# Optimization experiments

Measured on AMD Instinct MI355X. Metric: run time of the kernel, lower is better.

The kernel has to match this reference:

```python
import jax, jax.numpy as jnp
import numpy as np

B, DIM, H, W = 8, 256, 128, 128
HEADS = 4
C = DIM // HEADS  # per-head channels = 64


def conv1x1(x, w):
    # x: [b,c,h,w], w: [o,c] -> [b,o,h,w]
    return jnp.einsum('bchw,oc->bohw', x, w)


def setup_inputs() -> dict:
    key = jax.random.key(0)
    ks = jax.random.split(key, 10)
    d3 = DIM * 3
    return {
        'x': jax.random.normal(ks[0], (B, DIM, H, W), dtype=jnp.float32),
        'w_qkv': jax.random.normal(ks[1], (d3, DIM), dtype=jnp.float32) * (1.0 / np.sqrt(DIM)),
        'w_dw': jax.random.normal(ks[2], (d3, 1, 3, 3), dtype=jnp.float32) * (1.0 / 3.0),
        'temperature': jnp.ones((HEADS, 1, 1), dtype=jnp.float32),
        'attn1': jnp.array([0.2], dtype=jnp.float32),
        'attn2': jnp.array([0.2], dtype=jnp.float32),
        'attn3': jnp.array([0.2], dtype=jnp.float32),
        'attn4': jnp.array([0.2], dtype=jnp.float32),
        'gate_w1': jax.random.normal(ks[3], (DIM // 2, DIM), dtype=jnp.float32) * (1.0 / np.sqrt(DIM)),
        'gate_b1': jnp.zeros((DIM // 2,), dtype=jnp.float32),
        'gate_w2': jax.random.normal(ks[4], (1, DIM // 2), dtype=jnp.float32) * (1.0 / np.sqrt(DIM // 2)),
        'gate_b2': jnp.zeros((1,), dtype=jnp.float32),
    }


def reference(x, w_qkv, w_dw, temperature, attn1, attn2, attn3, attn4,
              gate_w1, gate_b1, gate_w2, gate_b2):
    b, c, h, w = x.shape
    n = h * w
    # qkv: 1x1 conv then 3x3 depthwise conv (groups = 3*dim)
    qkv = conv1x1(x, w_qkv)
    qkv = jax.lax.conv_general_dilated(
        qkv, w_dw, window_strides=(1, 1), padding='SAME',
        feature_group_count=3 * DIM,
        dimension_numbers=('NCHW', 'OIHW', 'NCHW'))
    q, k, v = jnp.split(qkv, 3, axis=1)
    # b (head c) h w -> b head c (h w)
    q = q.reshape(b, HEADS, C, n)
    k = k.reshape(b, HEADS, C, n)
    v = v.reshape(b, HEADS, C, n)
    # L2 normalize along token dim (F.normalize, eps=1e-12)
    q = q / jnp.maximum(jnp.linalg.norm(q, axis=-1, keepdims=True), 1e-12)
    k = k / jnp.maximum(jnp.linalg.norm(k, axis=-1, keepdims=True), 1e-12)
    # gate -> dynamic_k = int(C * mean(sigmoid(...)))
    g = jax.nn.relu(conv1x1(x, gate_w1) + gate_b1[None, :, None, None])
    g = jax.nn.sigmoid(conv1x1(g, gate_w2) + gate_b2[None, :, None, None])
    dk = jnp.clip(jnp.floor(C * jnp.mean(g)).astype(jnp.int32), 1, C)
    # channel attention: [b, heads, C, C]
    attn = jnp.einsum('bhcn,bhdn->bhcd', q, k) * temperature[None]
    # top-k mask: keep entries >= dk-th largest per row (ties negligible)
    vals = jax.lax.top_k(attn, C)[0]  # descending sorted values
    thresh = vals[..., dk - 1][..., None]
    attn = jnp.where(attn >= thresh, attn, -jnp.inf)
    attn = jax.nn.softmax(attn, axis=-1)
    # out1..out4 are identical (attn @ v); dedup into one matmul
    av = jnp.einsum('bhcd,bhdn->bhcn', attn, v)
    out = av * (attn1 + attn2 + attn3 + attn4)
    return out.reshape(b, c, h, w)
```

## Files before the change

kernel.cpp:

```cpp
#include <hip/hip_runtime.h>
#include <hip/hip_bf16.h>
#include <cmath>

#define HW_ 16384
#define IMG_W 128
#define IMG_H 128
#define DIM_ 256
#define D3_ 768
#define HEADS_ 4
#define C_ 64
#define B_ 8

typedef unsigned short ushort_t;
typedef __attribute__((ext_vector_type(8))) short short8v;
typedef __attribute__((ext_vector_type(16))) float f32x16;

#define GLL16(gp, lp) __builtin_amdgcn_global_load_lds( \
    (const __attribute__((address_space(1))) void*)(gp), \
    (__attribute__((address_space(3))) void*)(lp), 16, 0, 0)

static __device__ __forceinline__ ushort_t f2bf_bits(float v) {
  __hip_bfloat16 h = __float2bfloat16(v);
  return *reinterpret_cast<ushort_t*>(&h);
}
static __device__ __forceinline__ float bf2f(ushort_t u) {
  return __uint_as_float(((unsigned int)u) << 16);
}

__global__ __launch_bounds__(256) void k0_wsplit(
    const float* __restrict__ wqkv, const float* __restrict__ gw1,
    ushort_t* __restrict__ WH, ushort_t* __restrict__ WL)
{
  const int row = blockIdx.x;
  const int t = threadIdx.x;
  const float* src = (row < 768) ? (wqkv + (size_t)row * DIM_)
                                 : (gw1 + (size_t)(row - 768) * DIM_);
  const float v = src[t];
  const ushort_t hb = f2bf_bits(v);
  WH[(size_t)row * DIM_ + t] = hb;
  WL[(size_t)row * DIM_ + t] = f2bf_bits(v - bf2f(hb));
}

__global__ __launch_bounds__(256, 2) void k1_mfma(
    const ushort_t* __restrict__ WH, const ushort_t* __restrict__ WL,
    const float* __restrict__ x, const float* __restrict__ gb1,
    const float* __restrict__ gw2, const float* __restrict__ gb2,
    float* __restrict__ qkvraw, float* __restrict__ gpart, int bbase)
{
  const int t = threadIdx.x;
  const int cb = blockIdx.x, rb = blockIdx.y, s = blockIdx.z;
  const int row0 = rb * 128, col0 = cb * 128;
  const float* xb = x + (size_t)(bbase + s) * DIM_ * HW_;

  __shared__ __align__(16) unsigned char lds[65536];
  ushort_t* ldsA = (ushort_t*)lds;
  float*    ldsB = (float*)(lds + 32768);

  const int lane = t & 63, wid = t >> 6;
  const int rr = lane & 31, lh = lane >> 5;

  const size_t arowb = (size_t)(row0 + wid * 32 + rr) * DIM_;

  f32x16 acc[4];
#pragma unroll
  for (int mi = 0; mi < 4; ++mi)
#pragma unroll
    for (int r = 0; r < 16; ++r) acc[mi][r] = 0.f;

  auto STAGE = [&](int pb, int kt) {
    ushort_t* abase = ldsA + pb * 8192;
#pragma unroll
    for (int i = 0; i < 2; ++i) {
      const int koff = kt * 32 + i * 16 + lh * 8;
      ushort_t* dst = abase + (wid * 2 + i) * 512;
      GLL16(WH + arowb + koff, dst);
      GLL16(WL + arowb + koff, dst + 4096);
    }
    float* bbase = ldsB + pb * 4096;
#pragma unroll
    for (int j = 0; j < 4; ++j) {
      const int crow = wid * 8 + j * 2 + lh;
      const float* src = xb + (size_t)(kt * 32 + crow) * HW_ + col0 + rr * 4;
      GLL16(src, bbase + (wid * 8 + j * 2) * 128);
    }
  };

  auto COMPUTE = [&](int pb) {
    const ushort_t* pAH = ldsA + pb * 8192;
    const ushort_t* pAL = pAH + 4096;
    const float* bx = ldsB + pb * 4096;
    const int lo = lane * 8;
    const int pidx = wid * 32 + rr;
#pragma unroll
    for (int ks = 0; ks < 2; ++ks) {
      short8v ah[4], al[4];
#pragma unroll
      for (int mi = 0; mi < 4; ++mi) {
        const int base = mi * 1024 + ks * 512 + lo;
        ah[mi] = *(const short8v*)(pAH + base);
        al[mi] = *(const short8v*)(pAL + base);
      }
      short8v bh, bl;
#pragma unroll
      for (int j = 0; j < 8; ++j) {
        const float fv = bx[(ks * 16 + lh * 8 + j) * 128 + pidx];
        const ushort_t hb = f2bf_bits(fv);
        bh[j] = (short)hb;
        bl[j] = (short)f2bf_bits(fv - bf2f(hb));
      }
#pragma unroll
      for (int mi = 0; mi < 4; ++mi) {
        acc[mi] = __builtin_amdgcn_mfma_f32_32x32x16_bf16(ah[mi], bh, acc[mi], 0, 0, 0);
        acc[mi] = __builtin_amdgcn_mfma_f32_32x32x16_bf16(ah[mi], bl, acc[mi], 0, 0, 0);
        acc[mi] = __builtin_amdgcn_mfma_f32_32x32x16_bf16(al[mi], bh, acc[mi], 0, 0, 0);
      }
    }
  };

  STAGE(0, 0);
  __syncthreads();

  for (int kt = 0; kt < 8; ++kt) {
    const int pb = kt & 1;
    if (kt < 7) STAGE(pb ^ 1, kt + 1);
    COMPUTE(pb);
    __syncthreads();
  }

  const int cl = lane & 31;
  if (rb < 6) {
    const int p = col0 + wid * 32 + cl;
#pragma unroll
    for (int mi = 0; mi < 4; ++mi)
#pragma unroll
      for (int r = 0; r < 16; ++r) {
        const int row = (r & 3) + 8 * (r >> 2) + 4 * lh;
        const int m = row0 + mi * 32 + row;
        qkvraw[((size_t)s * D3_ + m) * HW_ + p] = acc[mi][r];
      }
  } else {
    float ps = 0.f;
#pragma unroll
    for (int mi = 0; mi < 4; ++mi)
#pragma unroll
      for (int r = 0; r < 16; ++r) {
        const int row = (r & 3) + 8 * (r >> 2) + 4 * lh;
        const int gr = mi * 32 + row;
        ps += fmaxf(acc[mi][r] + gb1[gr], 0.f) * gw2[gr];
      }
    ps += __shfl_xor(ps, 32, 64);
    float* sred = (float*)lds;
    float* red2 = sred + 128;
    if (lh == 0) sred[wid * 32 + cl] = ps;
    __syncthreads();
    float sig = 0.f;
    if (t < 128) {
      const float sv = sred[t] + gb2[0];
      sig = 1.f / (1.f + expf(-sv));
    }
    __syncthreads();
    red2[t] = sig;
    __syncthreads();
    for (int o = 128; o > 0; o >>= 1) {
      if (t < o) red2[t] += red2[t + o];
      __syncthreads();
    }
    if (t == 0) gpart[(size_t)(bbase + s) * 128 + cb] = red2[0];
  }
}

__global__ __launch_bounds__(256) void k3a_dw(
    const float* __restrict__ qkvraw, const float* __restrict__ wdw,
    float* __restrict__ uni, float* __restrict__ vout,
    float* __restrict__ ssq_part, int bbase)
{
  const int t = threadIdx.x;
  const int ytile = blockIdx.x;
  const int ch = blockIdx.y;
  const int s = blockIdx.z;
  const int b = bbase + s;
  const int y0 = ytile * 32;
  float* qdw = uni + (size_t)s * 512 * HW_;
  float* kdw = qdw + (size_t)DIM_ * HW_;

  __shared__ float sm[34][130];
  const float* in = qkvraw + ((size_t)s * D3_ + ch) * HW_;

  if (t < 34) { sm[t][0] = 0.f; sm[t][129] = 0.f; }
#pragma unroll 2
  for (int i = t; i < 1088; i += 256) {
    const int r = i >> 5;
    const int xq = (i & 31) << 2;
    const int row = y0 - 1 + r;
    float4 v = make_float4(0.f, 0.f, 0.f, 0.f);
    if (row >= 0 && row < IMG_H)
      v = *(const float4*)(in + row * IMG_W + xq);
    sm[r][1 + xq] = v.x; sm[r][2 + xq] = v.y;
    sm[r][3 + xq] = v.z; sm[r][4 + xq] = v.w;
  }
  const float* wp = wdw + ch * 9;
  const float w00 = wp[0], w01 = wp[1], w02 = wp[2],
              w10 = wp[3], w11 = wp[4], w12 = wp[5],
              w20 = wp[6], w21 = wp[7], w22 = wp[8];
  __syncthreads();

  float* outp;
  if (ch < 256)       outp = qdw + (size_t)ch * HW_;
  else if (ch < 512)  outp = kdw + (size_t)(ch - 256) * HW_;
  else                outp = vout + ((size_t)b * DIM_ + (ch - 512)) * HW_;

  float sq = 0.f;
#pragma unroll
  for (int it = 0; it < 16; ++it) {
    const int px = t + it * 256;
    const int yl = px >> 7, xx = px & 127;
    const float a =
      w00 * sm[yl][xx]     + w01 * sm[yl][xx + 1]     + w02 * sm[yl][xx + 2] +
      w10 * sm[yl + 1][xx] + w11 * sm[yl + 1][xx + 1] + w12 * sm[yl + 1][xx + 2] +
      w20 * sm[yl + 2][xx] + w21 * sm[yl + 2][xx + 1] + w22 * sm[yl + 2][xx + 2];
    outp[y0 * IMG_W + px] = a;
    sq += a * a;
  }

  if (ch < 512) {
    __shared__ float red[256];
    red[t] = sq;
    __syncthreads();
    for (int o = 128; o > 0; o >>= 1) {
      if (t < o) red[t] += red[t + o];
      __syncthreads();
    }
    if (t == 0) ssq_part[((size_t)b * 512 + ch) * 4 + ytile] = red[0];
  }
}

__global__ __launch_bounds__(256) void k3b_gram(
    const float* __restrict__ uni, float* __restrict__ S_part, int bbase)
{
  const int t = threadIdx.x;
  const int chunk = blockIdx.x;
  const int h = blockIdx.y;
  const int s = blockIdx.z;
  const int b = bbase + s;
  const int p0 = chunk * 512;
  const float* qdw = uni + (size_t)s * 512 * HW_;
  const float* kdw = qdw + (size_t)DIM_ * HW_;

  __shared__ float qs[64][68];
  __shared__ float ks[64][68];

  const int rc = t >> 4, dc = t & 15;

  float acc[4][4];
#pragma unroll
  for (int i = 0; i < 4; ++i)
#pragma unroll
    for (int j = 0; j < 4; ++j) acc[i][j] = 0.f;

  const float* qbase = qdw + (size_t)h * 64 * HW_ + p0;
  const float* kbase = kdw + (size_t)h * 64 * HW_ + p0;

  for (int kk = 0; kk < 512; kk += 64) {
    __syncthreads();
#pragma unroll
    for (int j = 0; j < 4; ++j) {
      const int lin = t + j * 256;
      const int c = lin >> 4;
      const int px0 = (lin & 15) << 2;
      const float4 qv = *(const float4*)(qbase + (size_t)c * HW_ + kk + px0);
      const float4 kv = *(const float4*)(kbase + (size_t)c * HW_ + kk + px0);
      qs[px0 + 0][c] = qv.x; qs[px0 + 1][c] = qv.y;
      qs[px0 + 2][c] = qv.z; qs[px0 + 3][c] = qv.w;
      ks[px0 + 0][c] = kv.x; ks[px0 + 1][c] = kv.y;
      ks[px0 + 2][c] = kv.z; ks[px0 + 3][c] = kv.w;
    }
    __syncthreads();
#pragma unroll 4
    for (int p = 0; p < 64; ++p) {
      const float4 q4 = *(const float4*)&qs[p][rc * 4];
      const float4 k4 = *(const float4*)&ks[p][dc * 4];
      const float qa[4] = {q4.x, q4.y, q4.z, q4.w};
      const float ka[4] = {k4.x, k4.y, k4.z, k4.w};
#pragma unroll
      for (int i = 0; i < 4; ++i)
#pragma unroll
        for (int jj = 0; jj < 4; ++jj) acc[i][jj] += qa[i] * ka[jj];
    }
  }
  float* op = S_part + (((size_t)(b * HEADS_ + h)) * 32 + chunk) * 4096;
#pragma unroll
  for (int i = 0; i < 4; ++i) {
    float4 v;
    v.x = acc[i][0]; v.y = acc[i][1]; v.z = acc[i][2]; v.w = acc[i][3];
    *(float4*)(op + (rc * 4 + i) * 64 + dc * 4) = v;
  }
}

__global__ __launch_bounds__(256) void k3c_reduce(
    const float* __restrict__ S_part, float* __restrict__ S)
{
  const int t = threadIdx.x;
  const int bh = blockIdx.y;
  const int e = blockIdx.x * 256 + t;
  float sum = 0.f;
#pragma unroll 8
  for (int c = 0; c < 32; ++c)
    sum += S_part[((size_t)bh * 32 + c) * 4096 + e];
  S[(size_t)bh * 4096 + e] = sum;
}

__global__ __launch_bounds__(256) void k4_final(
    const float* __restrict__ S, const float* __restrict__ ssq_part,
    const float* __restrict__ gpart, const float* __restrict__ temperature,
    const float* __restrict__ a1, const float* __restrict__ a2,
    const float* __restrict__ a3, const float* __restrict__ a4,
    float* __restrict__ attn)
{
  const int t = threadIdx.x;
  const int lane = t & 63, w = t >> 6;
  const int bh = blockIdx.x;
  const int b = bh >> 2, h = bh & 3;

  __shared__ float red[256];
  __shared__ float invq[64], invk[64];

  red[t] = gpart[t] + gpart[t + 256] + gpart[t + 512] + gpart[t + 768];
  __syncthreads();
  for (int o = 128; o > 0; o >>= 1) {
    if (t < o) red[t] += red[t + o];
    __syncthreads();
  }
  const float mean = red[0] / (float)((size_t)B_ * HW_);
  int dk = (int)floorf((float)C_ * mean);
  dk = min(max(dk, 1), 64);

  if (t < 128) {
    const int d = t & 63;
    const int ch = (t < 64 ? 0 : 256) + h * 64 + d;
    const float* pp = ssq_part + ((size_t)b * 512 + ch) * 4;
    const float sv = pp[0] + pp[1] + pp[2] + pp[3];
    const float inv = 1.f / fmaxf(sqrtf(sv), 1e-12f);
    if (t < 64) invq[d] = inv; else invk[d] = inv;
  }
  __syncthreads();

  const float tval = temperature[h];
  const float ascale = a1[0] + a2[0] + a3[0] + a4[0];
  const float* Sp = S + (size_t)bh * 4096;
  float* op = attn + (size_t)bh * 4096;

  for (int i = 0; i < 16; ++i) {
    const int c = w * 16 + i;
    const float val = Sp[c * 64 + lane] * invq[c] * invk[lane] * tval;
    int rank = 0;
    for (int j = 0; j < 64; ++j) {
      const float vj = __shfl(val, j, 64);
      rank += ((vj > val) || (vj == val && j < lane)) ? 1 : 0;
    }
    const bool keep = rank < dk;
    float mv = keep ? val : -INFINITY;
#pragma unroll
    for (int m = 1; m < 64; m <<= 1) mv = fmaxf(mv, __shfl_xor(mv, m, 64));
    const float e = keep ? expf(val - mv) : 0.f;
    float ssum = e;
#pragma unroll
    for (int m = 1; m < 64; m <<= 1) ssum += __shfl_xor(ssum, m, 64);
    op[c * 64 + lane] = (e / ssum) * ascale;
  }
}

__global__ __launch_bounds__(256) void k5_av(
    const float* __restrict__ attn, float* __restrict__ out)
{
  const int t = threadIdx.x;
  const int pc = blockIdx.x;
  const int h = blockIdx.y;
  const int b = blockIdx.z;
  const int p0 = pc * 128;

  __shared__ float vs[64][128];
  __shared__ float As5[64][64];

  const float* ap = attn + ((size_t)(b * HEADS_ + h)) * 4096;
  float* As5f = &As5[0][0];
#pragma unroll
  for (int j = 0; j < 4; ++j) {
    const int idx = t * 4 + j * 1024;
    *(float4*)&As5f[idx] = *(const float4*)(ap + idx);
  }

  float* base = out + ((size_t)b * DIM_ + h * 64) * HW_ + p0;
#pragma unroll
  for (int k = 0; k < 8; ++k) {
    const int fi = (t + k * 256) * 4;
    const int r = fi >> 7, c = fi & 127;
    *(float4*)&vs[r][c] = *(const float4*)(base + (size_t)r * HW_ + c);
  }
  __syncthreads();

  const int px4 = (t & 31) * 4;
  const int ch0 = (t >> 5) * 8;

  float4 acc[8];
#pragma unroll
  for (int ci = 0; ci < 8; ++ci) acc[ci] = make_float4(0.f, 0.f, 0.f, 0.f);

#pragma unroll 4
  for (int d = 0; d < 64; ++d) {
    const float4 v4 = *(const float4*)&vs[d][px4];
#pragma unroll
    for (int ci = 0; ci < 8; ++ci) {
      const float a = As5[ch0 + ci][d];
      acc[ci].x = fmaf(a, v4.x, acc[ci].x);
      acc[ci].y = fmaf(a, v4.y, acc[ci].y);
      acc[ci].z = fmaf(a, v4.z, acc[ci].z);
      acc[ci].w = fmaf(a, v4.w, acc[ci].w);
    }
  }

#pragma unroll
  for (int ci = 0; ci < 8; ++ci)
    *(float4*)(base + (size_t)(ch0 + ci) * HW_ + px4) = acc[ci];
}

extern "C" void kernel_launch(void* const* d_in, const int* in_sizes, int n_in,
                              void* d_out, int out_size, void* d_ws, size_t ws_size,
                              hipStream_t stream)
{
  const float* x    = (const float*)d_in[0];
  const float* wqkv = (const float*)d_in[1];
  const float* wdw  = (const float*)d_in[2];
  const float* temp = (const float*)d_in[3];
  const float* a1   = (const float*)d_in[4];
  const float* a2   = (const float*)d_in[5];
  const float* a3   = (const float*)d_in[6];
  const float* a4   = (const float*)d_in[7];
  const float* gw1  = (const float*)d_in[8];
  const float* gb1  = (const float*)d_in[9];
  const float* gw2  = (const float*)d_in[10];
  const float* gb2  = (const float*)d_in[11];
  float* out = (float*)d_out;
  (void)in_sizes; (void)n_in; (void)out_size;

  const size_t HWs = (size_t)HW_;
  const size_t perb_f = (size_t)1280 * HWs;
  const size_t fixed_f = (size_t)32 * 32 * 4096
                       + (size_t)32 * 4096
                       + (size_t)8 * 512 * 4
                       + 1024
                       + (size_t)32 * 4096
                       + (size_t)2 * 896 * 256 / 2 + 64;
  int NB = 8;
  while (NB > 1) {
    if ((perb_f * (size_t)NB + fixed_f) * 4 <= ws_size) break;
    NB >>= 1;
  }

  float* ws = (float*)d_ws;
  size_t off = 0;
  float* qkvraw = ws + off; off += (size_t)NB * D3_ * HWs;
  float* uni    = ws + off; off += (size_t)NB * 512 * HWs;
  float* S_part = ws + off; off += (size_t)32 * 32 * 4096;
  float* S      = ws + off; off += (size_t)32 * 4096;
  float* ssqp   = ws + off; off += (size_t)8 * 512 * 4;
  float* gpart  = ws + off; off += 1024;
  float* attnb  = ws + off; off += (size_t)32 * 4096;
  ushort_t* WH  = (ushort_t*)(ws + off);
  ushort_t* WL  = WH + (size_t)896 * 256;

  k0_wsplit<<<dim3(896), 256, 0, stream>>>(wqkv, gw1, WH, WL);

  for (int g = 0; g < B_ / NB; ++g) {
    const int bbase = g * NB;
    k1_mfma<<<dim3(128, 7, NB), 256, 0, stream>>>(WH, WL, x, gb1, gw2, gb2,
                                                  qkvraw, gpart, bbase);
    k3a_dw<<<dim3(4, 768, NB), 256, 0, stream>>>(qkvraw, wdw, uni, out, ssqp, bbase);
    k3b_gram<<<dim3(32, 4, NB), 256, 0, stream>>>(uni, S_part, bbase);
  }
  k3c_reduce<<<dim3(16, 32), 256, 0, stream>>>(S_part, S);
  k4_final<<<dim3(32), 256, 0, stream>>>(S, ssqp, gpart, temp, a1, a2, a3, a4, attnb);
  k5_av<<<dim3(128, 4, 8), 256, 0, stream>>>(attnb, out);
}
```

Measured before the change: 628.9 us.

## Overlap next-batch QKV GEMM with Gram via merged kernel; fold reduce into final

```diff
diff --git a/kernel.cpp b/kernel.cpp
--- a/kernel.cpp
+++ b/kernel.cpp
@@ -41,18 +41,16 @@
   WL[(size_t)row * DIM_ + t] = f2bf_bits(v - bf2f(hb));
 }
 
-__global__ __launch_bounds__(256, 2) void k1_mfma(
+__device__ __forceinline__ void k1_body(
+    unsigned char* lds, int t, int cb, int rb, int s,
     const ushort_t* __restrict__ WH, const ushort_t* __restrict__ WL,
     const float* __restrict__ x, const float* __restrict__ gb1,
     const float* __restrict__ gw2, const float* __restrict__ gb2,
     float* __restrict__ qkvraw, float* __restrict__ gpart, int bbase)
 {
-  const int t = threadIdx.x;
-  const int cb = blockIdx.x, rb = blockIdx.y, s = blockIdx.z;
   const int row0 = rb * 128, col0 = cb * 128;
   const float* xb = x + (size_t)(bbase + s) * DIM_ * HW_;
 
-  __shared__ __align__(16) unsigned char lds[65536];
   ushort_t* ldsA = (ushort_t*)lds;
   float*    ldsB = (float*)(lds + 32768);
 
@@ -76,12 +74,12 @@
       GLL16(WH + arowb + koff, dst);
       GLL16(WL + arowb + koff, dst + 4096);
     }
-    float* bbase = ldsB + pb * 4096;
+    float* bbase2 = ldsB + pb * 4096;
 #pragma unroll
     for (int j = 0; j < 4; ++j) {
       const int crow = wid * 8 + j * 2 + lh;
       const float* src = xb + (size_t)(kt * 32 + crow) * HW_ + col0 + rr * 4;
-      GLL16(src, bbase + (wid * 8 + j * 2) * 128);
+      GLL16(src, bbase2 + (wid * 8 + j * 2) * 128);
     }
   };
 
@@ -166,6 +164,110 @@
       __syncthreads();
     }
     if (t == 0) gpart[(size_t)(bbase + s) * 128 + cb] = red2[0];
+  }
+}
+
+__device__ __forceinline__ void k3b_body(
+    float (*qs)[68], float (*ks)[68], int t, int chunk, int h, int s, int b,
+    const float* __restrict__ uni, float* __restrict__ S_part)
+{
+  const int p0 = chunk * 512;
+  const float* qdw = uni + (size_t)s * 512 * HW_;
+  const float* kdw = qdw + (size_t)DIM_ * HW_;
+
+  const int rc = t >> 4, dc = t & 15;
+
+  float acc[4][4];
+#pragma unroll
+  for (int i = 0; i < 4; ++i)
+#pragma unroll
+    for (int j = 0; j < 4; ++j) acc[i][j] = 0.f;
+
+  const float* qbase = qdw + (size_t)h * 64 * HW_ + p0;
+  const float* kbase = kdw + (size_t)h * 64 * HW_ + p0;
+
+  for (int kk = 0; kk < 512; kk += 64) {
+    __syncthreads();
+#pragma unroll
+    for (int j = 0; j < 4; ++j) {
+      const int lin = t + j * 256;
+      const int c = lin >> 4;
+      const int px0 = (lin & 15) << 2;
+      const float4 qv = *(const float4*)(qbase + (size_t)c * HW_ + kk + px0);
+      const float4 kv = *(const float4*)(kbase + (size_t)c * HW_ + kk + px0);
+      qs[px0 + 0][c] = qv.x; qs[px0 + 1][c] = qv.y;
+      qs[px0 + 2][c] = qv.z; qs[px0 + 3][c] = qv.w;
+      ks[px0 + 0][c] = kv.x; ks[px0 + 1][c] = kv.y;
+      ks[px0 + 2][c] = kv.z; ks[px0 + 3][c] = kv.w;
+    }
+    __syncthreads();
+#pragma unroll 4
+    for (int p = 0; p < 64; ++p) {
+      const float4 q4 = *(const float4*)&qs[p][rc * 4];
+      const float4 k4 = *(const float4*)&ks[p][dc * 4];
+      const float qa[4] = {q4.x, q4.y, q4.z, q4.w};
+      const float ka[4] = {k4.x, k4.y, k4.z, k4.w};
+#pragma unroll
+      for (int i = 0; i < 4; ++i)
+#pragma unroll
+        for (int jj = 0; jj < 4; ++jj) acc[i][jj] += qa[i] * ka[jj];
+    }
+  }
+  float* op = S_part + (((size_t)(b * HEADS_ + h)) * 32 + chunk) * 4096;
+#pragma unroll
+  for (int i = 0; i < 4; ++i) {
+    float4 v;
+    v.x = acc[i][0]; v.y = acc[i][1]; v.z = acc[i][2]; v.w = acc[i][3];
+    *(float4*)(op + (rc * 4 + i) * 64 + dc * 4) = v;
+  }
+}
+
+__global__ __launch_bounds__(256, 2) void k1_mfma(
+    const ushort_t* __restrict__ WH, const ushort_t* __restrict__ WL,
+    const float* __restrict__ x, const float* __restrict__ gb1,
+    const float* __restrict__ gw2, const float* __restrict__ gb2,
+    float* __restrict__ qkvraw, float* __restrict__ gpart, int bbase)
+{
+  __shared__ __align__(16) unsigned char lds[65536];
+  k1_body(lds, threadIdx.x, blockIdx.x, blockIdx.y, blockIdx.z,
+          WH, WL, x, gb1, gw2, gb2, qkvraw, gpart, bbase);
+}
+
+__global__ __launch_bounds__(256, 2) void k3b_gram(
+    const float* __restrict__ uni, float* __restrict__ S_part, int bbase)
+{
+  __shared__ float qs[64][68];
+  __shared__ float ks[64][68];
+  k3b_body(qs, ks, threadIdx.x, blockIdx.x, blockIdx.y, blockIdx.z,
+           bbase + blockIdx.z, uni, S_part);
+}
+
+__global__ __launch_bounds__(256, 2) void k_uber(
+    const ushort_t* __restrict__ WH, const ushort_t* __restrict__ WL,
+    const float* __restrict__ x, const float* __restrict__ gb1,
+    const float* __restrict__ gw2, const float* __restrict__ gb2,
+    float* __restrict__ qkvraw, float* __restrict__ gpart,
+    const float* __restrict__ uni, float* __restrict__ S_part,
+    int nb, int bbase_k3b, int bbase_k1)
+{
+  __shared__ __align__(16) unsigned char lds[65536];
+  const int t = threadIdx.x;
+  const int nk3b = nb * 128;
+  int bid = blockIdx.x;
+  if (bid < nk3b) {
+    const int chunk = bid & 31;
+    const int h = (bid >> 5) & 3;
+    const int s = bid >> 7;
+    float (*qs)[68] = (float(*)[68])lds;
+    float (*ks)[68] = (float(*)[68])(lds + 64 * 68 * sizeof(float));
+    k3b_body(qs, ks, t, chunk, h, s, bbase_k3b + s, uni, S_part);
+  } else {
+    bid -= nk3b;
+    const int cb = bid & 127;
+    const int r = bid >> 7;
+    const int rb = r % 7;
+    const int s = r / 7;
+    k1_body(lds, t, cb, rb, s, WH, WL, x, gb1, gw2, gb2, qkvraw, gpart, bbase_k1);
   }
 }
 
@@ -234,83 +336,8 @@
   }
 }
 
-__global__ __launch_bounds__(256) void k3b_gram(
-    const float* __restrict__ uni, float* __restrict__ S_part, int bbase)
-{
-  const int t = threadIdx.x;
-  const int chunk = blockIdx.x;
-  const int h = blockIdx.y;
-  const int s = blockIdx.z;
-  const int b = bbase + s;
-  const int p0 = chunk * 512;
-  const float* qdw = uni + (size_t)s * 512 * HW_;
-  const float* kdw = qdw + (size_t)DIM_ * HW_;
-
-  __shared__ float qs[64][68];
-  __shared__ float ks[64][68];
-
-  const int rc = t >> 4, dc = t & 15;
-
-  float acc[4][4];
-#pragma unroll
-  for (int i = 0; i < 4; ++i)
-#pragma unroll
-    for (int j = 0; j < 4; ++j) acc[i][j] = 0.f;
-
-  const float* qbase = qdw + (size_t)h * 64 * HW_ + p0;
-  const float* kbase = kdw + (size_t)h * 64 * HW_ + p0;
-
-  for (int kk = 0; kk < 512; kk += 64) {
-    __syncthreads();
-#pragma unroll
-    for (int j = 0; j < 4; ++j) {
-      const int lin = t + j * 256;
-      const int c = lin >> 4;
-      const int px0 = (lin & 15) << 2;
-      const float4 qv = *(const float4*)(qbase + (size_t)c * HW_ + kk + px0);
-      const float4 kv = *(const float4*)(kbase + (size_t)c * HW_ + kk + px0);
-      qs[px0 + 0][c] = qv.x; qs[px0 + 1][c] = qv.y;
-      qs[px0 + 2][c] = qv.z; qs[px0 + 3][c] = qv.w;
-      ks[px0 + 0][c] = kv.x; ks[px0 + 1][c] = kv.y;
-      ks[px0 + 2][c] = kv.z; ks[px0 + 3][c] = kv.w;
-    }
-    __syncthreads();
-#pragma unroll 4
-    for (int p = 0; p < 64; ++p) {
-      const float4 q4 = *(const float4*)&qs[p][rc * 4];
-      const float4 k4 = *(const float4*)&ks[p][dc * 4];
-      const float qa[4] = {q4.x, q4.y, q4.z, q4.w};
-      const float ka[4] = {k4.x, k4.y, k4.z, k4.w};
-#pragma unroll
-      for (int i = 0; i < 4; ++i)
-#pragma unroll
-        for (int jj = 0; jj < 4; ++jj) acc[i][jj] += qa[i] * ka[jj];
-    }
-  }
-  float* op = S_part + (((size_t)(b * HEADS_ + h)) * 32 + chunk) * 4096;
-#pragma unroll
-  for (int i = 0; i < 4; ++i) {
-    float4 v;
-    v.x = acc[i][0]; v.y = acc[i][1]; v.z = acc[i][2]; v.w = acc[i][3];
-    *(float4*)(op + (rc * 4 + i) * 64 + dc * 4) = v;
-  }
-}
-
-__global__ __launch_bounds__(256) void k3c_reduce(
-    const float* __restrict__ S_part, float* __restrict__ S)
-{
-  const int t = threadIdx.x;
-  const int bh = blockIdx.y;
-  const int e = blockIdx.x * 256 + t;
-  float sum = 0.f;
-#pragma unroll 8
-  for (int c = 0; c < 32; ++c)
-    sum += S_part[((size_t)bh * 32 + c) * 4096 + e];
-  S[(size_t)bh * 4096 + e] = sum;
-}
-
 __global__ __launch_bounds__(256) void k4_final(
-    const float* __restrict__ S, const float* __restrict__ ssq_part,
+    const float* __restrict__ S_part, const float* __restrict__ ssq_part,
     const float* __restrict__ gpart, const float* __restrict__ temperature,
     const float* __restrict__ a1, const float* __restrict__ a2,
     const float* __restrict__ a3, const float* __restrict__ a4,
@@ -321,8 +348,18 @@
   const int bh = blockIdx.x;
   const int b = bh >> 2, h = bh & 3;
 
+  __shared__ float Ss[4096];
   __shared__ float red[256];
   __shared__ float invq[64], invk[64];
+
+  for (int i = 0; i < 16; ++i) {
+    const int e = i * 256 + t;
+    float sum = 0.f;
+#pragma unroll 8
+    for (int c = 0; c < 32; ++c)
+      sum += S_part[((size_t)bh * 32 + c) * 4096 + e];
+    Ss[e] = sum;
+  }
 
   red[t] = gpart[t] + gpart[t + 256] + gpart[t + 512] + gpart[t + 768];
   __syncthreads();
@@ -346,12 +383,11 @@
 
   const float tval = temperature[h];
   const float ascale = a1[0] + a2[0] + a3[0] + a4[0];
-  const float* Sp = S + (size_t)bh * 4096;
   float* op = attn + (size_t)bh * 4096;
 
   for (int i = 0; i < 16; ++i) {
     const int c = w * 16 + i;
-    const float val = Sp[c * 64 + lane] * invq[c] * invk[lane] * tval;
+    const float val = Ss[c * 64 + lane] * invq[c] * invk[lane] * tval;
     int rank = 0;
     for (int j = 0; j < 64; ++j) {
       const float vj = __shfl(val, j, 64);
@@ -445,7 +481,6 @@
   const size_t HWs = (size_t)HW_;
   const size_t perb_f = (size_t)1280 * HWs;
   const size_t fixed_f = (size_t)32 * 32 * 4096
-                       + (size_t)32 * 4096
                        + (size_t)8 * 512 * 4
                        + 1024
                        + (size_t)32 * 4096
@@ -461,7 +496,6 @@
   float* qkvraw = ws + off; off += (size_t)NB * D3_ * HWs;
   float* uni    = ws + off; off += (size_t)NB * 512 * HWs;
   float* S_part = ws + off; off += (size_t)32 * 32 * 4096;
-  float* S      = ws + off; off += (size_t)32 * 4096;
   float* ssqp   = ws + off; off += (size_t)8 * 512 * 4;
   float* gpart  = ws + off; off += 1024;
   float* attnb  = ws + off; off += (size_t)32 * 4096;
@@ -470,14 +504,22 @@
 
   k0_wsplit<<<dim3(896), 256, 0, stream>>>(wqkv, gw1, WH, WL);
 
-  for (int g = 0; g < B_ / NB; ++g) {
+  const int G = B_ / NB;
+  for (int g = 0; g < G; ++g) {
     const int bbase = g * NB;
-    k1_mfma<<<dim3(128, 7, NB), 256, 0, stream>>>(WH, WL, x, gb1, gw2, gb2,
-                                                  qkvraw, gpart, bbase);
+    if (g == 0)
+      k1_mfma<<<dim3(128, 7, NB), 256, 0, stream>>>(WH, WL, x, gb1, gw2, gb2,
+                                                    qkvraw, gpart, bbase);
     k3a_dw<<<dim3(4, 768, NB), 256, 0, stream>>>(qkvraw, wdw, uni, out, ssqp, bbase);
-    k3b_gram<<<dim3(32, 4, NB), 256, 0, stream>>>(uni, S_part, bbase);
-  }
-  k3c_reduce<<<dim3(16, 32), 256, 0, stream>>>(S_part, S);
-  k4_final<<<dim3(32), 256, 0, stream>>>(S, ssqp, gpart, temp, a1, a2, a3, a4, attnb);
+    if (g + 1 < G) {
+      k_uber<<<dim3(NB * 1024), 256, 0, stream>>>(
+          WH, WL, x, gb1, gw2, gb2, qkvraw, gpart, uni, S_part,
+          NB, bbase, bbase + NB);
+    } else {
+      k3b_gram<<<dim3(32, 4, NB), 256, 0, stream>>>(uni, S_part, bbase);
+    }
+  }
+  k4_final<<<dim3(32), 256, 0, stream>>>(S_part, ssqp, gpart, temp,
+                                         a1, a2, a3, a4, attnb);
   k5_av<<<dim3(128, 4, 8), 256, 0, stream>>>(attnb, out);
 }
```

After: 658.5 us. +4.7%, slower.
